# Optimization experiments

Hardware: AMD Instinct MI355X
Metric: run time of the kernel (lower is better)

The kernel has to match this reference:

```python
import jax, jax.numpy as jnp
import numpy as np

D = 256      # wsi_projection_dim / SNN hidden
E = 1024     # wsi_embedding_dim
N = 60000    # num WSI patches
H = 8        # n_heads
DH = D // H  # head dim
K = 3        # int(6 * topk_ratio)
SIZES = (100, 200, 300, 400, 500, 600)
NC = 4       # num_classes
EPS = 1e-5


def _ln(x, g, b):
    m = x.mean(-1, keepdims=True)
    v = ((x - m) ** 2).mean(-1, keepdims=True)
    return (x - m) / jnp.sqrt(v + EPS) * g + b


def setup_inputs() -> dict:
    key = jax.random.key(0)
    ks = iter(jax.random.split(key, 64))
    sc = 0.02
    inp = {}
    inp["x_path"] = jax.random.normal(next(ks), (1, N, E), dtype=jnp.float32)
    for i, s in enumerate(SIZES):
        inp[f"x_omic{i+1}"] = jax.random.normal(next(ks), (s,), dtype=jnp.float32)
    # per-pathway SNN blocks: Linear(size,256)+ELU, Linear(256,256)+ELU
    for i, s in enumerate(SIZES):
        inp[f"sw1_{i}"] = sc * jax.random.normal(next(ks), (s, D), dtype=jnp.float32)
    inp["sb1"] = jnp.zeros((len(SIZES), D), jnp.float32)
    inp["sw2"] = sc * jax.random.normal(next(ks), (len(SIZES), D, D), dtype=jnp.float32)
    inp["sb2"] = jnp.zeros((len(SIZES), D), jnp.float32)
    # wsi projection
    inp["wp"] = sc * jax.random.normal(next(ks), (E, D), dtype=jnp.float32)
    inp["bp"] = jnp.zeros((D,), jnp.float32)
    # gene attention MLP 256->64->1
    inp["wa1"] = sc * jax.random.normal(next(ks), (D, 64), dtype=jnp.float32)
    inp["ba1"] = jnp.zeros((64,), jnp.float32)
    inp["wa2"] = sc * jax.random.normal(next(ks), (64, 1), dtype=jnp.float32)
    inp["ba2"] = jnp.zeros((1,), jnp.float32)
    # MultiheadAttention projections
    for nm in ("wq", "wk", "wv", "wo"):
        inp[nm] = sc * jax.random.normal(next(ks), (D, D), dtype=jnp.float32)
    for nm in ("bq", "bk", "bv", "bo"):
        inp[nm] = jnp.zeros((D,), jnp.float32)
    inp["ln1_g"] = jnp.ones((D,), jnp.float32)
    inp["ln1_b"] = jnp.zeros((D,), jnp.float32)
    # bilinear fusion 512->256->256
    inp["wf1"] = sc * jax.random.normal(next(ks), (2 * D, D), dtype=jnp.float32)
    inp["bf1"] = jnp.zeros((D,), jnp.float32)
    inp["wf2"] = sc * jax.random.normal(next(ks), (D, D), dtype=jnp.float32)
    inp["bf2"] = jnp.zeros((D,), jnp.float32)
    inp["ln2_g"] = jnp.ones((D,), jnp.float32)
    inp["ln2_b"] = jnp.zeros((D,), jnp.float32)
    inp["wc"] = sc * jax.random.normal(next(ks), (D, NC), dtype=jnp.float32)
    inp["bc"] = jnp.zeros((NC,), jnp.float32)
    return inp


def _forward(x_path, x_omics, sw1s, sb1, sw2, sb2, wp, bp, wa1, ba1, wa2, ba2,
             wq, bq, wk, bk, wv, bv, wo, bo, ln1_g, ln1_b,
             wf1, bf1, wf2, bf2, ln2_g, ln2_b, wc, bc):
    # per-pathway SNN (eval: AlphaDropout = identity)
    h = [jax.nn.elu(jax.nn.elu(x @ w1 + sb1[i]) @ sw2[i] + sb2[i])
         for i, (x, w1) in enumerate(zip(x_omics, sw1s))]
    bag = jnp.stack(h)[None]                      # [1, G, D]
    # gene selection: softmax -> topk -> gather (mask*gather == gather)
    scores = (jax.nn.relu(bag @ wa1 + ba1) @ wa2 + ba2)[..., 0]   # [1, G]
    attw = jax.nn.softmax(scores, axis=1)
    _, idx = jax.lax.top_k(attw, K)               # [1, K]
    selected = jnp.take_along_axis(bag, idx[..., None], axis=1)  # [1, K, D]
    # wsi projection (eval: Dropout = identity)
    wsi = jax.nn.relu(x_path @ wp + bp)           # [1, N, D]
    # cross-attention: queries = selected genes, keys/values = wsi patches
    q = (selected @ wq + bq).reshape(1, K, H, DH).transpose(0, 2, 1, 3)
    k_ = (wsi @ wk + bk).reshape(1, N, H, DH).transpose(0, 2, 1, 3)
    v_ = (wsi @ wv + bv).reshape(1, N, H, DH).transpose(0, 2, 1, 3)
    att = jax.nn.softmax(jnp.einsum('bhqd,bhkd->bhqk', q, k_) / np.float32(np.sqrt(DH)), axis=-1)
    attn_out = jnp.einsum('bhqk,bhkd->bhqd', att, v_).transpose(0, 2, 1, 3).reshape(1, K, D)
    attn_out = attn_out @ wo + bo                 # [1, K, D]
    # adaptive_avg_pool2d over N -> K bins (N divisible by K -> equal bins)
    pooled = wsi.reshape(1, K, N // K, D).mean(axis=2)  # [1, K, D]
    attended = _ln(attn_out + pooled, ln1_g, ln1_b)
    attended_mean = attended.mean(axis=1)         # [1, D]
    gene_features = selected.mean(axis=1)         # [1, D]
    comb = jnp.concatenate([attended_mean, gene_features], axis=1)  # [1, 2D]
    f = jax.nn.relu(comb @ wf1 + bf1)
    f = jax.nn.relu(f @ wf2 + bf2)
    fused = _ln(f + attended_mean, ln2_g, ln2_b)
    return fused @ wc + bc                        # [1, num_classes]


def reference(x_path, x_omic1, x_omic2, x_omic3, x_omic4, x_omic5, x_omic6,
              sw1_0, sw1_1, sw1_2, sw1_3, sw1_4, sw1_5, sb1, sw2, sb2,
              wp, bp, wa1, ba1, wa2, ba2,
              wq, bq, wk, bk, wv, bv, wo, bo, ln1_g, ln1_b,
              wf1, bf1, wf2, bf2, ln2_g, ln2_b, wc, bc):
    x_omics = (x_omic1, x_omic2, x_omic3, x_omic4, x_omic5, x_omic6)
    sw1s = (sw1_0, sw1_1, sw1_2, sw1_3, sw1_4, sw1_5)
    return _forward(x_path, x_omics, sw1s, sb1, sw2, sb2, wp, bp, wa1, ba1, wa2, ba2,
                    wq, bq, wk, bk, wv, bv, wo, bo, ln1_g, ln1_b,
                    wf1, bf1, wf2, bf2, ln2_g, ln2_b, wc, bc)
```

## Files before the change

### kernel.cpp

```cpp
#include <hip/hip_runtime.h>
#include <hip/hip_bf16.h>
#include <math.h>

typedef unsigned short ushort_t;
typedef __attribute__((ext_vector_type(8))) short bf16x8;
typedef __attribute__((ext_vector_type(4))) float f32x4;

#define NB 512
#define NBLK 469
#define TP 128
#define NHQ 24
#define LN_EPS 1e-5f

#define WS_BAG 0
#define WS_SEL 1536
#define WS_GENE 2304
#define WS_PM 3584
#define WS_PL (WS_PM + NB*NHQ)
#define WS_PACC (WS_PL + NB*NHQ)
#define WS_PPOOL (WS_PACC + NB*768)
#define WS_ATTN (WS_PPOOL + NB*768)
#define WS_POOLED (WS_ATTN + 768)
#define WS_BF16 (WS_POOLED + 768)
#define U_WPT 0
#define U_WKT 262144
#define U_WVT 327680
#define U_QB  393216

__device__ __forceinline__ ushort_t f2bf(float f) {
    __hip_bfloat16 h = __float2bfloat16(f);
    return *reinterpret_cast<ushort_t*>(&h);
}
__device__ __forceinline__ float bf2f(unsigned int u) {
    union { unsigned int i; float f; } c; c.i = u << 16; return c.f;
}
__device__ __forceinline__ unsigned int pk2(float a, float b) {
    return (unsigned int)f2bf(a) | ((unsigned int)f2bf(b) << 16);
}

__global__ void prep_kernel(const float* __restrict__ wp, const float* __restrict__ wk,
                            const float* __restrict__ wv, ushort_t* __restrict__ ub) {
    const int b = blockIdx.x, t = threadIdx.x;
    if (b < 16) {
        const int D16 = b;
        for (int i = 0; i < 64; ++i) {
            int f = t + i * 256;
            int K32 = f >> 9, r = f & 511;
            int lg = r >> 7, lm2 = (r >> 3) & 15, e = r & 7;
            int k = K32 * 32 + lg * 8 + e, d = D16 * 16 + lm2;
            ub[U_WPT + D16 * 16384 + f] = f2bf(wp[(size_t)k * 256 + d]);
        }
    } else if (b < 32) {
        const int D16 = b - 16;
        for (int i = 0; i < 16; ++i) {
            int f = t + i * 256;
            int K32 = f >> 9, r = f & 511;
            int lg = r >> 7, lm2 = (r >> 3) & 15, e = r & 7;
            int k = K32 * 32 + lg * 8 + e, d = D16 * 16 + lm2;
            ub[U_WKT + D16 * 4096 + f] = f2bf(wk[(size_t)k * 256 + d]);
        }
    } else {
        const int D16 = b - 32;
        for (int i = 0; i < 16; ++i) {
            int f = t + i * 256;
            int K32 = f >> 9, r = f & 511;
            int lg = r >> 7, lm2 = (r >> 3) & 15, e = r & 7;
            int k = K32 * 32 + lg * 8 + e, d = D16 * 16 + lm2;
            ub[U_WVT + D16 * 4096 + f] = f2bf(wv[(size_t)k * 256 + d]);
        }
    }
}

struct PrepArgs {
    const float* xo[6];
    const float* w1[6];
    int sz[6];
};

__global__ void snn_kernel(PrepArgs pa, const float* __restrict__ sb1,
                           const float* __restrict__ sw2, const float* __restrict__ sb2,
                           float* __restrict__ bag) {
    __shared__ float xsh[600];
    __shared__ float t1sh[256];
    const int i = blockIdx.x;
    const int t = threadIdx.x;
    const int s = pa.sz[i];
    const float* xo = pa.xo[i];
    const float* w1 = pa.w1[i];
    for (int j = t; j < s; j += 256) xsh[j] = xo[j];
    __syncthreads();
    float acc = sb1[i * 256 + t];
    for (int j = 0; j < s; ++j) acc += xsh[j] * w1[j * 256 + t];
    t1sh[t] = acc > 0.f ? acc : expm1f(acc);
    __syncthreads();
    float acc2 = sb2[i * 256 + t];
    const float* w2 = sw2 + (size_t)i * 256 * 256;
    for (int j = 0; j < 256; ++j) acc2 += t1sh[j] * w2[j * 256 + t];
    bag[i * 256 + t] = acc2 > 0.f ? acc2 : expm1f(acc2);
}

__global__ void select_kernel(const float* __restrict__ wa1, const float* __restrict__ ba1,
                              const float* __restrict__ wa2, const float* __restrict__ ba2,
                              const float* __restrict__ wq, const float* __restrict__ bq,
                              float* __restrict__ wsf, ushort_t* __restrict__ ub) {
    __shared__ float bsh[6][256];
    __shared__ float ysh[64];
    __shared__ float ssh[8];
    __shared__ int isel[3];
    const int t = threadIdx.x;
    for (int j = t; j < 1536; j += 256) ((float*)bsh)[j] = wsf[WS_BAG + j];
    __syncthreads();
    for (int i = 0; i < 6; ++i) {
        if (t < 64) {
            float acc = ba1[t];
            for (int j = 0; j < 256; ++j) acc += bsh[i][j] * wa1[j * 64 + t];
            ysh[t] = fmaxf(acc, 0.f) * wa2[t];
        }
        __syncthreads();
        if (t == 0) {
            float sc = ba2[0];
            for (int j = 0; j < 64; ++j) sc += ysh[j];
            ssh[i] = sc;
        }
        __syncthreads();
    }
    if (t == 0) {
        float sc[6];
        for (int i = 0; i < 6; ++i) sc[i] = ssh[i];
        for (int k = 0; k < 3; ++k) {
            int best = 0; float bv = sc[0];
            for (int i = 1; i < 6; ++i) if (sc[i] > bv) { bv = sc[i]; best = i; }
            isel[k] = best;
            sc[best] = -INFINITY;
        }
    }
    __syncthreads();
    float g = 0.f;
    for (int k = 0; k < 3; ++k) {
        float v = bsh[isel[k]][t];
        wsf[WS_SEL + k * 256 + t] = v;
        g += v;
    }
    wsf[WS_GENE + t] = g * (1.f / 3.f);
    for (int kq = 0; kq < 3; ++kq) {
        float acc = bq[t];
        const float* srow = bsh[isel[kq]];
        for (int j = 0; j < 256; ++j) acc += srow[j] * wq[j * 256 + t];
        float v = acc * 0.17677669529663687f;
        int hq = (t >> 5) * 3 + kq, dd = t & 31;
        ub[U_QB + hq * 32 + dd] = f2bf(v);
    }
}

#define LOAD_X(xr, c) { \
    _Pragma("unroll") for (int i_ = 0; i_ < 4; ++i_) { \
        int f_ = tid + i_ * 512; int p_ = f_ >> 4, c4_ = f_ & 15; \
        if (n0 + p_ < 60000) \
            xr[i_] = *(const float4*)(xp + (size_t)(n0 + p_) * 1024 + (c) * 64 + c4_ * 4); \
        else { xr[i_].x = 0.f; xr[i_].y = 0.f; xr[i_].z = 0.f; xr[i_].w = 0.f; } } }

#define STORE_X(xr) { \
    _Pragma("unroll") for (int i_ = 0; i_ < 4; ++i_) { \
        int f_ = tid + i_ * 512; int p_ = f_ >> 4, c4_ = f_ & 15; \
        int byte_ = (p_ * 128 + c4_ * 8) ^ ((p_ & 7) << 4); \
        uint2 u_; u_.x = pk2(xr[i_].x, xr[i_].y); u_.y = pk2(xr[i_].z, xr[i_].w); \
        *(uint2*)((char*)x_s + byte_) = u_; } }

#define LOAD_W1(dst, c) { \
    _Pragma("unroll") for (int ks_ = 0; ks_ < 2; ++ks_) \
    _Pragma("unroll") for (int dt_ = 0; dt_ < 4; ++dt_) \
        dst[ks_ * 4 + dt_] = *(const bf16x8*)(wpP + ((size_t)(((w & 3) * 4 + dt_) * 32 + (c) * 2 + ks_)) * 512 + lane * 8); }

#define MFMA_CHUNK(wf) { \
    _Pragma("unroll") for (int ks_ = 0; ks_ < 2; ++ks_) { \
        bf16x8 bfr_[4]; \
        _Pragma("unroll") for (int pt_ = 0; pt_ < 4; ++pt_) { \
            int p_ = wp0 + pt_ * 16 + lm; \
            int byte_ = (p_ * 128 + ks_ * 64 + lg * 16) ^ ((p_ & 7) << 4); \
            bfr_[pt_] = *(const bf16x8*)((const char*)x_s + byte_); } \
        _Pragma("unroll") for (int dt_ = 0; dt_ < 4; ++dt_) \
        _Pragma("unroll") for (int pt_ = 0; pt_ < 4; ++pt_) \
            acc[dt_ * 4 + pt_] = __builtin_amdgcn_mfma_f32_16x16x32_bf16(wf[ks_ * 4 + dt_], bfr_[pt_], acc[dt_ * 4 + pt_], 0, 0, 0); } }

__global__ __launch_bounds__(512, 2) void main_kernel(
    const float* __restrict__ xp, const float* __restrict__ bp,
    const float* __restrict__ bk, const float* __restrict__ bv,
    const ushort_t* __restrict__ ub, float* __restrict__ wsf)
{
    __shared__ __align__(16) ushort_t wsi_s[128 * 256];
    __shared__ __align__(16) ushort_t kv_s[128 * 256];
    __shared__ __align__(16) ushort_t x_s[128 * 64];
    __shared__ __align__(16) ushort_t p_s[NHQ * 128];
    __shared__ float mlc_s[72];

    const int tid = threadIdx.x;
    const int b = blockIdx.x;
    const int lane = tid & 63;
    const int w = tid >> 6;
    const int lm = lane & 15;
    const int lg = lane >> 4;
    const int lmc = (lm < 3) ? lm : 2;
    const int wd0 = (w & 3) * 64;
    const int wp0 = (w >> 2) * 64;

    const ushort_t* wpP = ub + U_WPT;
    const ushort_t* wkP = ub + U_WKT;
    const ushort_t* wvP = ub + U_WVT;

    bf16x8 qfrag;
    if (lm < 3) qfrag = *(const bf16x8*)(ub + U_QB + (w * 3 + lm) * 32 + lg * 8);
    else { bf16x8 z = {0,0,0,0,0,0,0,0}; qfrag = z; }

    if (tid < 24) { mlc_s[tid] = -INFINITY; mlc_s[24 + tid] = 0.f; mlc_s[48 + tid] = 0.f; }

    f32x4 pv[2] = {{0.f,0.f,0.f,0.f},{0.f,0.f,0.f,0.f}};
    float pl0 = 0.f, pl1 = 0.f, pl2 = 0.f;
    __syncthreads();

    const int n0 = b * TP;
    {
        f32x4 acc[16];
#pragma unroll
        for (int i = 0; i < 16; ++i) acc[i] = (f32x4){0.f,0.f,0.f,0.f};

        float4 xr[4];
        bf16x8 wA[8], wB[8];
        LOAD_X(xr, 0); LOAD_W1(wA, 0);
        for (int c = 0; c < 16; c += 2) {
            __syncthreads();
            STORE_X(xr);
            __syncthreads();
            LOAD_X(xr, c + 1); LOAD_W1(wB, c + 1);
            MFMA_CHUNK(wA);
            __syncthreads();
            STORE_X(xr);
            __syncthreads();
            if (c + 2 < 16) { LOAD_X(xr, c + 2); LOAD_W1(wA, c + 2); }
            MFMA_CHUNK(wB);
        }
#pragma unroll
        for (int dt = 0; dt < 4; ++dt) {
            int d0 = wd0 + dt * 16 + lg * 4;
            float4 bb = *(const float4*)(bp + d0);
#pragma unroll
            for (int pt = 0; pt < 4; ++pt) {
                int p = wp0 + pt * 16 + lm;
                f32x4 v = acc[dt * 4 + pt];
                uint2 u;
                u.x = pk2(fmaxf(v[0] + bb.x, 0.f), fmaxf(v[1] + bb.y, 0.f));
                u.y = pk2(fmaxf(v[2] + bb.z, 0.f), fmaxf(v[3] + bb.w, 0.f));
                int byte = (p * 512 + d0 * 2) ^ ((p & 7) << 4);
                *(uint2*)((char*)wsi_s + byte) = u;
            }
        }
    }
    __syncthreads();

    {
        int d = tid & 255, half = tid >> 8;
#pragma unroll 16
        for (int pp = 0; pp < 64; ++pp) {
            int p = half * 64 + pp;
            int gp = n0 + p;
            int byte = (p * 512 + d * 2) ^ ((p & 7) << 4);
            float v = bf2f((unsigned int)*(const ushort_t*)((const char*)wsi_s + byte));
            pl0 += (gp < 20000) ? v : 0.f;
            pl1 += (gp >= 20000 && gp < 40000) ? v : 0.f;
            pl2 += (gp >= 40000 && gp < 60000) ? v : 0.f;
        }
    }

    {
        f32x4 acc2[16];
#pragma unroll
        for (int i = 0; i < 16; ++i) acc2[i] = (f32x4){0.f,0.f,0.f,0.f};
#pragma unroll
        for (int ks = 0; ks < 8; ++ks) {
            bf16x8 wf[4];
#pragma unroll
            for (int dt = 0; dt < 4; ++dt)
                wf[dt] = *(const bf16x8*)(wkP + ((size_t)(((w & 3) * 4 + dt) * 8 + ks)) * 512 + lane * 8);
            bf16x8 bfr[4];
#pragma unroll
            for (int pt = 0; pt < 4; ++pt) {
                int p = wp0 + pt * 16 + lm;
                int byte = (p * 512 + (ks * 32 + lg * 8) * 2) ^ ((p & 7) << 4);
                bfr[pt] = *(const bf16x8*)((const char*)wsi_s + byte);
            }
#pragma unroll
            for (int dt = 0; dt < 4; ++dt)
#pragma unroll
                for (int pt = 0; pt < 4; ++pt)
                    acc2[dt * 4 + pt] = __builtin_amdgcn_mfma_f32_16x16x32_bf16(wf[dt], bfr[pt], acc2[dt * 4 + pt], 0, 0, 0);
        }
#pragma unroll
        for (int dt = 0; dt < 4; ++dt) {
            int d0 = wd0 + dt * 16 + lg * 4;
            float4 bb = *(const float4*)(bk + d0);
#pragma unroll
            for (int pt = 0; pt < 4; ++pt) {
                int p = wp0 + pt * 16 + lm;
                f32x4 v = acc2[dt * 4 + pt];
                uint2 u;
                u.x = pk2(v[0] + bb.x, v[1] + bb.y);
                u.y = pk2(v[2] + bb.z, v[3] + bb.w);
                int byte = (p * 512 + d0 * 2) ^ ((p & 7) << 4);
                *(uint2*)((char*)kv_s + byte) = u;
            }
        }
    }
    __syncthreads();

    {
        f32x4 sc[8];
#pragma unroll
        for (int blk = 0; blk < 8; ++blk) {
            sc[blk] = (f32x4){0.f,0.f,0.f,0.f};
            int p = blk * 16 + lm;
            int byte = (p * 512 + (w * 32 + lg * 8) * 2) ^ ((p & 7) << 4);
            bf16x8 kf = *(const bf16x8*)((const char*)kv_s + byte);
            sc[blk] = __builtin_amdgcn_mfma_f32_16x16x32_bf16(kf, qfrag, sc[blk], 0, 0, 0);
        }
        float m_old = mlc_s[w * 3 + lmc];
        float tmax = -INFINITY;
#pragma unroll
        for (int blk = 0; blk < 8; ++blk)
#pragma unroll
            for (int j = 0; j < 4; ++j) {
                int p = blk * 16 + lg * 4 + j;
                if (n0 + p >= 60000) sc[blk][j] = -INFINITY;
                tmax = fmaxf(tmax, sc[blk][j]);
            }
        tmax = fmaxf(tmax, __shfl_xor(tmax, 16));
        tmax = fmaxf(tmax, __shfl_xor(tmax, 32));
        float mnew = fmaxf(m_old, tmax);
        float lsum = 0.f;
#pragma unroll
        for (int blk = 0; blk < 8; ++blk)
#pragma unroll
            for (int j = 0; j < 4; ++j) {
                float e = __expf(sc[blk][j] - mnew);
                sc[blk][j] = e;
                lsum += e;
            }
        lsum += __shfl_xor(lsum, 16);
        lsum += __shfl_xor(lsum, 32);
        float corr = __expf(m_old - mnew);
        if (lane < 3) {
            mlc_s[w * 3 + lane] = mnew;
            mlc_s[24 + w * 3 + lane] = mlc_s[24 + w * 3 + lane] * corr + lsum;
            mlc_s[48 + w * 3 + lane] = corr;
        }
        if (lm < 3) {
#pragma unroll
            for (int blk = 0; blk < 8; ++blk) {
                int p0 = blk * 16 + lg * 4;
                *(unsigned int*)(p_s + (w * 3 + lm) * 128 + p0) = pk2(sc[blk][0], sc[blk][1]);
                *(unsigned int*)(p_s + (w * 3 + lm) * 128 + p0 + 2) = pk2(sc[blk][2], sc[blk][3]);
            }
        }
    }
    __syncthreads();

    {
        f32x4 acc2[16];
#pragma unroll
        for (int i = 0; i < 16; ++i) acc2[i] = (f32x4){0.f,0.f,0.f,0.f};
#pragma unroll
        for (int ks = 0; ks < 8; ++ks) {
            bf16x8 wf[4];
#pragma unroll
            for (int dt = 0; dt < 4; ++dt)
                wf[dt] = *(const bf16x8*)(wvP + ((size_t)(((w & 3) * 4 + dt) * 8 + ks)) * 512 + lane * 8);
            bf16x8 bfr[4];
#pragma unroll
            for (int pt = 0; pt < 4; ++pt) {
                int p = wp0 + pt * 16 + lm;
                int byte = (p * 512 + (ks * 32 + lg * 8) * 2) ^ ((p & 7) << 4);
                bfr[pt] = *(const bf16x8*)((const char*)wsi_s + byte);
            }
#pragma unroll
            for (int dt = 0; dt < 4; ++dt)
#pragma unroll
                for (int pt = 0; pt < 4; ++pt)
                    acc2[dt * 4 + pt] = __builtin_amdgcn_mfma_f32_16x16x32_bf16(wf[dt], bfr[pt], acc2[dt * 4 + pt], 0, 0, 0);
        }
#pragma unroll
        for (int dt = 0; dt < 4; ++dt) {
            int d0 = wd0 + dt * 16 + lg * 4;
            float4 bb = *(const float4*)(bv + d0);
#pragma unroll
            for (int pt = 0; pt < 4; ++pt) {
                int p = wp0 + pt * 16 + lm;
                f32x4 v = acc2[dt * 4 + pt];
                float r[4] = {v[0] + bb.x, v[1] + bb.y, v[2] + bb.z, v[3] + bb.w};
#pragma unroll
                for (int j = 0; j < 4; ++j) {
                    int dd = d0 + j;
                    int byte = (dd * 256 + p * 2) ^ ((dd & 7) << 4);
                    *(ushort_t*)((char*)kv_s + byte) = f2bf(r[j]);
                }
            }
        }
    }
    __syncthreads();

    {
        float cj[4];
#pragma unroll
        for (int j = 0; j < 4; ++j) {
            int q = lg * 4 + j;
            cj[j] = mlc_s[48 + w * 3 + (q < 3 ? q : 2)];
        }
#pragma unroll
        for (int nb = 0; nb < 2; ++nb)
#pragma unroll
            for (int j = 0; j < 4; ++j) pv[nb][j] *= cj[j];
#pragma unroll
        for (int ks = 0; ks < 4; ++ks) {
            bf16x8 pa = *(const bf16x8*)(p_s + (w * 3 + lmc) * 128 + ks * 32 + lg * 8);
#pragma unroll
            for (int nb = 0; nb < 2; ++nb) {
                int row = w * 32 + nb * 16 + lm;
                int byte = (row * 256 + (ks * 32 + lg * 8) * 2) ^ ((row & 7) << 4);
                bf16x8 vb = *(const bf16x8*)((const char*)kv_s + byte);
                pv[nb] = __builtin_amdgcn_mfma_f32_16x16x32_bf16(pa, vb, pv[nb], 0, 0, 0);
            }
        }
    }

    __syncthreads();
    {
        float* scr = (float*)x_s;
        int d = tid & 255, half = tid >> 8;
        scr[half * 768 + 0 * 256 + d] = pl0;
        scr[half * 768 + 1 * 256 + d] = pl1;
        scr[half * 768 + 2 * 256 + d] = pl2;
    }
    __syncthreads();
    if (tid < 256) {
        float* scr = (float*)x_s;
#pragma unroll
        for (int bin = 0; bin < 3; ++bin)
            wsf[WS_PPOOL + b * 768 + bin * 256 + tid] = scr[bin * 256 + tid] + scr[768 + bin * 256 + tid];
    }
    if (tid < 24) {
        wsf[WS_PM + b * 24 + tid] = mlc_s[tid];
        wsf[WS_PL + b * 24 + tid] = mlc_s[24 + tid];
    }
    if (lg == 0) {
#pragma unroll
        for (int nb = 0; nb < 2; ++nb)
#pragma unroll
            for (int j = 0; j < 3; ++j) {
                int hq = w * 3 + j, dd = nb * 16 + lm;
                wsf[WS_PACC + b * 768 + hq * 32 + dd] = pv[nb][j];
            }
    }
}

__global__ void combine_kernel(float* __restrict__ wsf) {
    const int bidx = blockIdx.x;
    const int t = threadIdx.x;
    if (bidx < NHQ) {
        const int hq = bidx;
        float lmx = -INFINITY;
        for (int b = t; b < NBLK; b += 64) lmx = fmaxf(lmx, wsf[WS_PM + b * 24 + hq]);
#pragma unroll
        for (int o = 32; o > 0; o >>= 1) lmx = fmaxf(lmx, __shfl_xor(lmx, o));
        const float M = lmx;
        float L = 0.f;
        for (int b = t; b < NBLK; b += 64)
            L += wsf[WS_PL + b * 24 + hq] * __expf(wsf[WS_PM + b * 24 + hq] - M);
#pragma unroll
        for (int o = 32; o > 0; o >>= 1) L += __shfl_xor(L, o);
        const int dd = t & 31, half = t >> 5;
        float O = 0.f;
        for (int b = half; b < NBLK; b += 2)
            O += wsf[WS_PACC + b * 768 + hq * 32 + dd] * __expf(wsf[WS_PM + b * 24 + hq] - M);
        O += __shfl_xor(O, 32);
        if (t < 32) {
            int h = hq / 3, kq = hq - h * 3;
            wsf[WS_ATTN + kq * 256 + h * 32 + dd] = O / L;
        }
    } else {
        const int bin = bidx - NHQ;
        for (int rep = 0; rep < 4; ++rep) {
            int d = rep * 64 + t;
            float s = 0.f;
            for (int b = 0; b < NBLK; ++b) s += wsf[WS_PPOOL + b * 768 + bin * 256 + d];
            wsf[WS_POOLED + bin * 256 + d] = s * (1.f / 20000.f);
        }
    }
}

__device__ __forceinline__ float block_sum256(float v, float* red, int t) {
#pragma unroll
    for (int o = 32; o > 0; o >>= 1) v += __shfl_xor(v, o);
    if ((t & 63) == 0) red[t >> 6] = v;
    __syncthreads();
    float r = red[0] + red[1] + red[2] + red[3];
    __syncthreads();
    return r;
}

__global__ void final_kernel(const float* __restrict__ wo, const float* __restrict__ bo,
                             const float* __restrict__ ln1g, const float* __restrict__ ln1b,
                             const float* __restrict__ wf1, const float* __restrict__ bf1,
                             const float* __restrict__ wf2, const float* __restrict__ bf2,
                             const float* __restrict__ ln2g, const float* __restrict__ ln2b,
                             const float* __restrict__ wc, const float* __restrict__ bc,
                             float* __restrict__ wsf, float* __restrict__ out) {
    __shared__ float attnC[3][256];
    __shared__ float att[3][256];
    __shared__ float amean[256];
    __shared__ float gf[256];
    __shared__ float f1[256];
    __shared__ float red[256];
    const int t = threadIdx.x;
    for (int j = t; j < 768; j += 256) ((float*)attnC)[j] = wsf[WS_ATTN + j];
    gf[t] = wsf[WS_GENE + t];
    __syncthreads();
    for (int kq = 0; kq < 3; ++kq) {
        float acc = bo[t];
        for (int j = 0; j < 256; ++j) acc += attnC[kq][j] * wo[j * 256 + t];
        float x = acc + wsf[WS_POOLED + kq * 256 + t];
        float m = block_sum256(x, red, t) * (1.f / 256.f);
        float dv = x - m;
        float var = block_sum256(dv * dv, red, t) * (1.f / 256.f);
        att[kq][t] = dv * rsqrtf(var + LN_EPS) * ln1g[t] + ln1b[t];
    }
    __syncthreads();
    amean[t] = (att[0][t] + att[1][t] + att[2][t]) * (1.f / 3.f);
    __syncthreads();
    {
        float acc = bf1[t];
        for (int j = 0; j < 256; ++j) acc += amean[j] * wf1[j * 256 + t];
        for (int j = 0; j < 256; ++j) acc += gf[j] * wf1[(256 + j) * 256 + t];
        f1[t] = fmaxf(acc, 0.f);
    }
    __syncthreads();
    float acc2 = bf2[t];
    for (int j = 0; j < 256; ++j) acc2 += f1[j] * wf2[j * 256 + t];
    float y = fmaxf(acc2, 0.f) + amean[t];
    float m2 = block_sum256(y, red, t) * (1.f / 256.f);
    float dv2 = y - m2;
    float v2 = block_sum256(dv2 * dv2, red, t) * (1.f / 256.f);
    float fused = dv2 * rsqrtf(v2 + LN_EPS) * ln2g[t] + ln2b[t];
    red[t] = fused;
    __syncthreads();
    if (t < 4) {
        float o = bc[t];
        for (int j = 0; j < 256; ++j) o += red[j] * wc[j * 4 + t];
        out[t] = o;
    }
}

extern "C" void kernel_launch(void* const* d_in, const int* in_sizes, int n_in,
                              void* d_out, int out_size, void* d_ws, size_t ws_size,
                              hipStream_t stream) {
    const float* xp = (const float*)d_in[0];
    PrepArgs pa;
    for (int i = 0; i < 6; ++i) {
        pa.xo[i] = (const float*)d_in[1 + i];
        pa.w1[i] = (const float*)d_in[7 + i];
        pa.sz[i] = in_sizes[1 + i];
    }
    const float* sb1 = (const float*)d_in[13];
    const float* sw2 = (const float*)d_in[14];
    const float* sb2 = (const float*)d_in[15];
    const float* wp  = (const float*)d_in[16];
    const float* bp  = (const float*)d_in[17];
    const float* wa1 = (const float*)d_in[18];
    const float* ba1 = (const float*)d_in[19];
    const float* wa2 = (const float*)d_in[20];
    const float* ba2 = (const float*)d_in[21];
    const float* wq  = (const float*)d_in[22];
    const float* wk  = (const float*)d_in[23];
    const float* wv  = (const float*)d_in[24];
    const float* wo  = (const float*)d_in[25];
    const float* bq  = (const float*)d_in[26];
    const float* bk  = (const float*)d_in[27];
    const float* bv  = (const float*)d_in[28];
    const float* bo  = (const float*)d_in[29];
    const float* ln1g = (const float*)d_in[30];
    const float* ln1b = (const float*)d_in[31];
    const float* wf1 = (const float*)d_in[32];
    const float* bf1 = (const float*)d_in[33];
    const float* wf2 = (const float*)d_in[34];
    const float* bf2 = (const float*)d_in[35];
    const float* ln2g = (const float*)d_in[36];
    const float* ln2b = (const float*)d_in[37];
    const float* wc  = (const float*)d_in[38];
    const float* bc  = (const float*)d_in[39];

    float* wsf = (float*)d_ws;
    float* out = (float*)d_out;
    ushort_t* ub = (ushort_t*)(wsf + WS_BF16);

    prep_kernel<<<dim3(48), dim3(256), 0, stream>>>(wp, wk, wv, ub);
    snn_kernel<<<dim3(6), dim3(256), 0, stream>>>(pa, sb1, sw2, sb2, wsf + WS_BAG);
    select_kernel<<<dim3(1), dim3(256), 0, stream>>>(wa1, ba1, wa2, ba2, wq, bq, wsf, ub);
    main_kernel<<<dim3(NBLK), dim3(512), 0, stream>>>(xp, bp, bk, bv, ub, wsf);
    combine_kernel<<<dim3(27), dim3(64), 0, stream>>>(wsf);
    final_kernel<<<dim3(1), dim3(256), 0, stream>>>(wo, bo, ln1g, ln1b, wf1, bf1, wf2, bf2,
                                                    ln2g, ln2b, wc, bc, wsf, out);
}
```

Measured before the change: 740.6 us.

## Split fused projection/attention kernel into proj, attn and pool kernels

Replaces the single fused main kernel with three kernels: a projection GEMM that writes the ReLU'd bf16 WSI projection to workspace in an MFMA-friendly layout, an attention kernel over 64-patch tiles that computes K/V and partial softmax, and a separate pooling reduction. This aims to raise occupancy and parallelism, since the fused kernel had heavy register and LDS use and only 469 blocks. In exchange it adds a round trip of roughly 30 MB through global memory and more launches, and it runs only when the workspace is large enough. The LDS swizzle in the fallback path is also changed.

```diff
diff --git a/kernel.cpp b/kernel.cpp
--- a/kernel.cpp
+++ b/kernel.cpp
@@ -6,26 +6,28 @@
 typedef __attribute__((ext_vector_type(8))) short bf16x8;
 typedef __attribute__((ext_vector_type(4))) float f32x4;
 
-#define NB 512
-#define NBLK 469
-#define TP 128
 #define NHQ 24
 #define LN_EPS 1e-5f
+#define NBLK_F 469
+#define NBLK_A 938
+#define NPOOL 256
 
 #define WS_BAG 0
 #define WS_SEL 1536
 #define WS_GENE 2304
 #define WS_PM 3584
-#define WS_PL (WS_PM + NB*NHQ)
-#define WS_PACC (WS_PL + NB*NHQ)
-#define WS_PPOOL (WS_PACC + NB*768)
-#define WS_ATTN (WS_PPOOL + NB*768)
-#define WS_POOLED (WS_ATTN + 768)
-#define WS_BF16 (WS_POOLED + 768)
+#define WS_PL 28160
+#define WS_PACC 52736
+#define WS_PPOOL 839168
+#define WS_ATTN 1232384
+#define WS_POOLED 1233152
+#define WS_BF16 1233920
 #define U_WPT 0
 #define U_WKT 262144
 #define U_WVT 327680
 #define U_QB  393216
+#define U_WSIP 401408
+#define WS_SPLIT_BYTES 36474880ULL
 
 __device__ __forceinline__ ushort_t f2bf(float f) {
     __hip_bfloat16 h = __float2bfloat16(f);
@@ -152,6 +154,324 @@
     }
 }
 
+
+#define PLOAD_X(xr, c) { \
+    _Pragma("unroll") for (int i_ = 0; i_ < 4; ++i_) { \
+        int f_ = tid + i_ * 512; int p_ = f_ >> 4, c4_ = f_ & 15; \
+        if (n0 + p_ < 60000) \
+            xr[i_] = *(const float4*)(xp + (size_t)(n0 + p_) * 1024 + (c) * 64 + c4_ * 4); \
+        else { xr[i_].x = 0.f; xr[i_].y = 0.f; xr[i_].z = 0.f; xr[i_].w = 0.f; } } }
+
+#define PSTORE_X(xr, buf) { \
+    _Pragma("unroll") for (int i_ = 0; i_ < 4; ++i_) { \
+        int f_ = tid + i_ * 512; int p_ = f_ >> 4, c4_ = f_ & 15; \
+        int byte_ = (p_ * 128 + c4_ * 8) ^ ((p_ & 7) << 4); \
+        uint2 u_; u_.x = pk2(xr[i_].x, xr[i_].y); u_.y = pk2(xr[i_].z, xr[i_].w); \
+        *(uint2*)((buf) + byte_) = u_; } }
+
+__global__ __launch_bounds__(512, 4) void proj_kernel(
+    const float* __restrict__ xp, const float* __restrict__ bp,
+    const ushort_t* __restrict__ ub, ushort_t* __restrict__ wsiP)
+{
+    __shared__ __align__(16) char xbuf[2][16384];
+    const int tid = threadIdx.x;
+    const int b = blockIdx.x;
+    const int lane = tid & 63;
+    const int w = tid >> 6;
+    const int lm = lane & 15;
+    const int lg = lane >> 4;
+    const int wd0 = (w & 3) * 64;
+    const int n0 = b * 128;
+    const ushort_t* wpP = ub + U_WPT;
+
+    f32x4 acc[16];
+#pragma unroll
+    for (int i = 0; i < 16; ++i) acc[i] = (f32x4){0.f, 0.f, 0.f, 0.f};
+
+    float4 xr[4];
+    PLOAD_X(xr, 0);
+    PSTORE_X(xr, xbuf[0]);
+    PLOAD_X(xr, 1);
+    __syncthreads();
+#pragma unroll 1
+    for (int c = 0; c < 16; ++c) {
+        const char* cur = xbuf[c & 1];
+        if (c < 15) PSTORE_X(xr, xbuf[(c + 1) & 1]);
+        if (c < 14) PLOAD_X(xr, c + 2);
+#pragma unroll
+        for (int ks = 0; ks < 2; ++ks) {
+            bf16x8 wf[4];
+#pragma unroll
+            for (int dt = 0; dt < 4; ++dt)
+                wf[dt] = *(const bf16x8*)(wpP + ((size_t)(((w & 3) * 4 + dt) * 32 + c * 2 + ks)) * 512 + lane * 8);
+            bf16x8 bfr[4];
+#pragma unroll
+            for (int pt = 0; pt < 4; ++pt) {
+                int p = (w >> 2) * 64 + pt * 16 + lm;
+                int byte = (p * 128 + ks * 64 + lg * 16) ^ ((p & 7) << 4);
+                bfr[pt] = *(const bf16x8*)(cur + byte);
+            }
+#pragma unroll
+            for (int dt = 0; dt < 4; ++dt)
+#pragma unroll
+                for (int pt = 0; pt < 4; ++pt)
+                    acc[dt * 4 + pt] = __builtin_amdgcn_mfma_f32_16x16x32_bf16(wf[dt], bfr[pt], acc[dt * 4 + pt], 0, 0, 0);
+        }
+        __syncthreads();
+    }
+#pragma unroll
+    for (int dt = 0; dt < 4; ++dt) {
+        int d0 = wd0 + dt * 16 + lg * 4;
+        float4 bb = *(const float4*)(bp + d0);
+        int ks2 = d0 >> 5, lg2 = (d0 >> 3) & 3, e0 = d0 & 7;
+#pragma unroll
+        for (int pt = 0; pt < 4; ++pt) {
+            int p16 = b * 8 + (w >> 2) * 4 + pt;
+            f32x4 v = acc[dt * 4 + pt];
+            uint2 u;
+            u.x = pk2(fmaxf(v[0] + bb.x, 0.f), fmaxf(v[1] + bb.y, 0.f));
+            u.y = pk2(fmaxf(v[2] + bb.z, 0.f), fmaxf(v[3] + bb.w, 0.f));
+            *(uint2*)(wsiP + (size_t)((p16 * 8 + ks2) * 4 + lg2) * 128 + lm * 8 + e0) = u;
+        }
+    }
+}
+
+__global__ __launch_bounds__(256, 4) void attn_kernel(
+    const float* __restrict__ bk, const float* __restrict__ bv,
+    const ushort_t* __restrict__ ub, const ushort_t* __restrict__ wsiP,
+    float* __restrict__ wsf)
+{
+    __shared__ __align__(16) ushort_t kv_s[64 * 256];
+    __shared__ __align__(16) ushort_t p_s[24 * 64];
+    const int tid = threadIdx.x;
+    const int b = blockIdx.x;
+    const int lane = tid & 63, w = tid >> 6;
+    const int lm = lane & 15, lg = lane >> 4;
+    const int lmc = lm < 3 ? lm : 2;
+    const int n0 = b * 64;
+    const int wd0 = w * 64;
+    const ushort_t* wkP = ub + U_WKT;
+    const ushort_t* wvP = ub + U_WVT;
+
+    {
+        f32x4 acc[16];
+#pragma unroll
+        for (int i = 0; i < 16; ++i) acc[i] = (f32x4){0.f, 0.f, 0.f, 0.f};
+#pragma unroll
+        for (int ks = 0; ks < 8; ++ks) {
+            bf16x8 wf[4], bfr[4];
+#pragma unroll
+            for (int dt = 0; dt < 4; ++dt)
+                wf[dt] = *(const bf16x8*)(wkP + ((size_t)((w * 4 + dt) * 8 + ks)) * 512 + lane * 8);
+#pragma unroll
+            for (int pt = 0; pt < 4; ++pt)
+                bfr[pt] = *(const bf16x8*)(wsiP + (size_t)(((b * 4 + pt) * 8 + ks) * 4 + lg) * 128 + lm * 8);
+#pragma unroll
+            for (int dt = 0; dt < 4; ++dt)
+#pragma unroll
+                for (int pt = 0; pt < 4; ++pt)
+                    acc[dt * 4 + pt] = __builtin_amdgcn_mfma_f32_16x16x32_bf16(wf[dt], bfr[pt], acc[dt * 4 + pt], 0, 0, 0);
+        }
+#pragma unroll
+        for (int dt = 0; dt < 4; ++dt) {
+            int d0 = wd0 + dt * 16 + lg * 4;
+            float4 bb = *(const float4*)(bk + d0);
+#pragma unroll
+            for (int pt = 0; pt < 4; ++pt) {
+                int p = pt * 16 + lm;
+                f32x4 v = acc[dt * 4 + pt];
+                uint2 u;
+                u.x = pk2(v[0] + bb.x, v[1] + bb.y);
+                u.y = pk2(v[2] + bb.z, v[3] + bb.w);
+                int byte = (p * 512 + d0 * 2) ^ ((p & 7) << 4);
+                *(uint2*)((char*)kv_s + byte) = u;
+            }
+        }
+    }
+    __syncthreads();
+
+    float m_reg[2], l_reg[2];
+#pragma unroll
+    for (int hh = 0; hh < 2; ++hh) {
+        int h = w * 2 + hh;
+        bf16x8 qf;
+        if (lm < 3) qf = *(const bf16x8*)(ub + U_QB + (h * 3 + lm) * 32 + lg * 8);
+        else { bf16x8 z = {0,0,0,0,0,0,0,0}; qf = z; }
+        f32x4 sc[4];
+#pragma unroll
+        for (int blk = 0; blk < 4; ++blk) {
+            sc[blk] = (f32x4){0.f, 0.f, 0.f, 0.f};
+            int p = blk * 16 + lm;
+            int byte = (p * 512 + (h * 32 + lg * 8) * 2) ^ ((p & 7) << 4);
+            bf16x8 kf = *(const bf16x8*)((const char*)kv_s + byte);
+            sc[blk] = __builtin_amdgcn_mfma_f32_16x16x32_bf16(kf, qf, sc[blk], 0, 0, 0);
+        }
+        float tmax = -INFINITY;
+#pragma unroll
+        for (int blk = 0; blk < 4; ++blk)
+#pragma unroll
+            for (int j = 0; j < 4; ++j) {
+                int p = blk * 16 + lg * 4 + j;
+                if (n0 + p >= 60000) sc[blk][j] = -INFINITY;
+                tmax = fmaxf(tmax, sc[blk][j]);
+            }
+        tmax = fmaxf(tmax, __shfl_xor(tmax, 16));
+        tmax = fmaxf(tmax, __shfl_xor(tmax, 32));
+        float lsum = 0.f;
+#pragma unroll
+        for (int blk = 0; blk < 4; ++blk)
+#pragma unroll
+            for (int j = 0; j < 4; ++j) {
+                float e = __expf(sc[blk][j] - tmax);
+                sc[blk][j] = e;
+                lsum += e;
+            }
+        lsum += __shfl_xor(lsum, 16);
+        lsum += __shfl_xor(lsum, 32);
+        m_reg[hh] = tmax;
+        l_reg[hh] = lsum;
+        if (lm < 3) {
+#pragma unroll
+            for (int blk = 0; blk < 4; ++blk) {
+                int p0 = blk * 16 + lg * 4;
+                *(unsigned int*)(p_s + (h * 3 + lm) * 64 + p0) = pk2(sc[blk][0], sc[blk][1]);
+                *(unsigned int*)(p_s + (h * 3 + lm) * 64 + p0 + 2) = pk2(sc[blk][2], sc[blk][3]);
+            }
+        }
+    }
+    __syncthreads();
+
+    {
+        f32x4 acc[16];
+#pragma unroll
+        for (int i = 0; i < 16; ++i) acc[i] = (f32x4){0.f, 0.f, 0.f, 0.f};
+#pragma unroll
+        for (int ks = 0; ks < 8; ++ks) {
+            bf16x8 wf[4], bfr[4];
+#pragma unroll
+            for (int dt = 0; dt < 4; ++dt)
+                wf[dt] = *(const bf16x8*)(wvP + ((size_t)((w * 4 + dt) * 8 + ks)) * 512 + lane * 8);
+#pragma unroll
+            for (int pt = 0; pt < 4; ++pt)
+                bfr[pt] = *(const bf16x8*)(wsiP + (size_t)(((b * 4 + pt) * 8 + ks) * 4 + lg) * 128 + lm * 8);
+#pragma unroll
+            for (int dt = 0; dt < 4; ++dt)
+#pragma unroll
+                for (int pt = 0; pt < 4; ++pt)
+                    acc[dt * 4 + pt] = __builtin_amdgcn_mfma_f32_16x16x32_bf16(wf[dt], bfr[pt], acc[dt * 4 + pt], 0, 0, 0);
+        }
+        __syncthreads();
+#pragma unroll
+        for (int dt = 0; dt < 4; ++dt) {
+            int d0 = wd0 + dt * 16 + lg * 4;
+            float4 bb = *(const float4*)(bv + d0);
+#pragma unroll
+            for (int pt = 0; pt < 4; ++pt) {
+                int p = pt * 16 + lm;
+                f32x4 v = acc[dt * 4 + pt];
+                float r[4] = {v[0] + bb.x, v[1] + bb.y, v[2] + bb.z, v[3] + bb.w};
+#pragma unroll
+                for (int j = 0; j < 4; ++j) {
+                    int dd = d0 + j;
+                    int byte = (dd * 128 + p * 2) ^ ((dd & 7) << 4);
+                    *(ushort_t*)((char*)kv_s + byte) = f2bf(r[j]);
+                }
+            }
+        }
+    }
+    __syncthreads();
+
+    f32x4 pv[2][2];
+#pragma unroll
+    for (int hh = 0; hh < 2; ++hh)
+#pragma unroll
+        for (int nb = 0; nb < 2; ++nb) pv[hh][nb] = (f32x4){0.f, 0.f, 0.f, 0.f};
+#pragma unroll
+    for (int hh = 0; hh < 2; ++hh) {
+        int h = w * 2 + hh;
+#pragma unroll
+        for (int ks = 0; ks < 2; ++ks) {
+            bf16x8 pa = *(const bf16x8*)(p_s + (h * 3 + lmc) * 64 + ks * 32 + lg * 8);
+#pragma unroll
+            for (int nb = 0; nb < 2; ++nb) {
+                int row = h * 32 + nb * 16 + lm;
+                int byte = (row * 128 + (ks * 32 + lg * 8) * 2) ^ ((row & 7) << 4);
+                bf16x8 vb = *(const bf16x8*)((const char*)kv_s + byte);
+                pv[hh][nb] = __builtin_amdgcn_mfma_f32_16x16x32_bf16(pa, vb, pv[hh][nb], 0, 0, 0);
+            }
+        }
+    }
+
+    if (lg == 0) {
+#pragma unroll
+        for (int hh = 0; hh < 2; ++hh)
+#pragma unroll
+            for (int nb = 0; nb < 2; ++nb)
+#pragma unroll
+                for (int j = 0; j < 3; ++j) {
+                    int hq = (w * 2 + hh) * 3 + j;
+                    wsf[WS_PACC + b * 768 + hq * 32 + nb * 16 + lm] = pv[hh][nb][j];
+                }
+    }
+    if (lm < 3 && lg == 0) {
+#pragma unroll
+        for (int hh = 0; hh < 2; ++hh) {
+            int hq = (w * 2 + hh) * 3 + lm;
+            wsf[WS_PM + b * 24 + hq] = m_reg[hh];
+            wsf[WS_PL + b * 24 + hq] = l_reg[hh];
+        }
+    }
+}
+
+__global__ __launch_bounds__(256, 8) void pool_kernel(const ushort_t* __restrict__ wsiP,
+                                                      float* __restrict__ wsf) {
+    const int tid = threadIdx.x, b = blockIdx.x;
+    const int lane = tid & 63;
+    const int lm = lane & 15, lg = (lane >> 4) & 3;
+    const int ks = ((b * 4) + (tid >> 6)) & 7;
+    f32x4 s[3][2];
+#pragma unroll
+    for (int i = 0; i < 3; ++i) { s[i][0] = (f32x4){0,0,0,0}; s[i][1] = (f32x4){0,0,0,0}; }
+    for (int sl = b * 256 + tid; sl < 1921024; sl += 65536) {
+        int p16 = sl >> 9;
+        if (p16 >= 3750) continue;
+        uint4 u = *(const uint4*)(wsiP + (size_t)sl * 8);
+        int bin = (p16 >= 2500) ? 2 : (p16 >= 1250 ? 1 : 0);
+        f32x4 a, c;
+        a[0] = bf2f(u.x & 0xffffu); a[1] = bf2f(u.x >> 16);
+        a[2] = bf2f(u.y & 0xffffu); a[3] = bf2f(u.y >> 16);
+        c[0] = bf2f(u.z & 0xffffu); c[1] = bf2f(u.z >> 16);
+        c[2] = bf2f(u.w & 0xffffu); c[3] = bf2f(u.w >> 16);
+        s[bin][0] += a; s[bin][1] += c;
+    }
+#pragma unroll
+    for (int o = 1; o < 16; o <<= 1)
+#pragma unroll
+        for (int bin = 0; bin < 3; ++bin)
+#pragma unroll
+            for (int hv = 0; hv < 2; ++hv)
+#pragma unroll
+                for (int e = 0; e < 4; ++e)
+                    s[bin][hv][e] += __shfl_xor(s[bin][hv][e], o);
+    if (lm == 0) {
+        int dbase = ks * 32 + lg * 8;
+#pragma unroll
+        for (int bin = 0; bin < 3; ++bin)
+#pragma unroll
+            for (int hv = 0; hv < 2; ++hv)
+#pragma unroll
+                for (int e = 0; e < 4; ++e)
+                    wsf[WS_PPOOL + b * 768 + bin * 256 + dbase + hv * 4 + e] = s[bin][hv][e];
+    } else if (lm == 1) {
+        int dbase = (ks ^ 4) * 32 + lg * 8;
+#pragma unroll
+        for (int bin = 0; bin < 3; ++bin)
+#pragma unroll
+            for (int e = 0; e < 8; ++e)
+                wsf[WS_PPOOL + b * 768 + bin * 256 + dbase + e] = 0.f;
+    }
+}
+
 #define LOAD_X(xr, c) { \
     _Pragma("unroll") for (int i_ = 0; i_ < 4; ++i_) { \
         int f_ = tid + i_ * 512; int p_ = f_ >> 4, c4_ = f_ & 15; \
@@ -217,12 +537,11 @@
     float pl0 = 0.f, pl1 = 0.f, pl2 = 0.f;
     __syncthreads();
 
-    const int n0 = b * TP;
+    const int n0 = b * 128;
     {
         f32x4 acc[16];
 #pragma unroll
         for (int i = 0; i < 16; ++i) acc[i] = (f32x4){0.f,0.f,0.f,0.f};
-
         float4 xr[4];
         bf16x8 wA[8], wB[8];
         LOAD_X(xr, 0); LOAD_W1(wA, 0);
@@ -397,7 +716,7 @@
 #pragma unroll
                 for (int j = 0; j < 4; ++j) {
                     int dd = d0 + j;
-                    int byte = (dd * 256 + p * 2) ^ ((dd & 7) << 4);
+                    int byte = (dd * 256 + p * 2) ^ ((dd & 14) << 2);
                     *(ushort_t*)((char*)kv_s + byte) = f2bf(r[j]);
                 }
             }
@@ -422,7 +741,7 @@
 #pragma unroll
             for (int nb = 0; nb < 2; ++nb) {
                 int row = w * 32 + nb * 16 + lm;
-                int byte = (row * 256 + (ks * 32 + lg * 8) * 2) ^ ((row & 7) << 4);
+                int byte = (row * 256 + (ks * 32 + lg * 8) * 2) ^ ((row & 14) << 2);
                 bf16x8 vb = *(const bf16x8*)((const char*)kv_s + byte);
                 pv[nb] = __builtin_amdgcn_mfma_f32_16x16x32_bf16(pa, vb, pv[nb], 0, 0, 0);
             }
@@ -459,24 +778,24 @@
     }
 }
 
-__global__ void combine_kernel(float* __restrict__ wsf) {
+__global__ void combine_kernel(float* __restrict__ wsf, int nblk, int npool) {
     const int bidx = blockIdx.x;
     const int t = threadIdx.x;
     if (bidx < NHQ) {
         const int hq = bidx;
         float lmx = -INFINITY;
-        for (int b = t; b < NBLK; b += 64) lmx = fmaxf(lmx, wsf[WS_PM + b * 24 + hq]);
+        for (int b = t; b < nblk; b += 64) lmx = fmaxf(lmx, wsf[WS_PM + b * 24 + hq]);
 #pragma unroll
         for (int o = 32; o > 0; o >>= 1) lmx = fmaxf(lmx, __shfl_xor(lmx, o));
         const float M = lmx;
         float L = 0.f;
-        for (int b = t; b < NBLK; b += 64)
+        for (int b = t; b < nblk; b += 64)
             L += wsf[WS_PL + b * 24 + hq] * __expf(wsf[WS_PM + b * 24 + hq] - M);
 #pragma unroll
         for (int o = 32; o > 0; o >>= 1) L += __shfl_xor(L, o);
         const int dd = t & 31, half = t >> 5;
         float O = 0.f;
-        for (int b = half; b < NBLK; b += 2)
+        for (int b = half; b < nblk; b += 2)
             O += wsf[WS_PACC + b * 768 + hq * 32 + dd] * __expf(wsf[WS_PM + b * 24 + hq] - M);
         O += __shfl_xor(O, 32);
         if (t < 32) {
@@ -488,7 +807,7 @@
         for (int rep = 0; rep < 4; ++rep) {
             int d = rep * 64 + t;
             float s = 0.f;
-            for (int b = 0; b < NBLK; ++b) s += wsf[WS_PPOOL + b * 768 + bin * 256 + d];
+            for (int b = 0; b < npool; ++b) s += wsf[WS_PPOOL + b * 768 + bin * 256 + d];
             wsf[WS_POOLED + bin * 256 + d] = s * (1.f / 20000.f);
         }
     }
@@ -601,8 +920,17 @@
     prep_kernel<<<dim3(48), dim3(256), 0, stream>>>(wp, wk, wv, ub);
     snn_kernel<<<dim3(6), dim3(256), 0, stream>>>(pa, sb1, sw2, sb2, wsf + WS_BAG);
     select_kernel<<<dim3(1), dim3(256), 0, stream>>>(wa1, ba1, wa2, ba2, wq, bq, wsf, ub);
-    main_kernel<<<dim3(NBLK), dim3(512), 0, stream>>>(xp, bp, bk, bv, ub, wsf);
-    combine_kernel<<<dim3(27), dim3(64), 0, stream>>>(wsf);
+
+    if (ws_size >= WS_SPLIT_BYTES) {
+        ushort_t* wsiP = ub + U_WSIP;
+        proj_kernel<<<dim3(NBLK_F), dim3(512), 0, stream>>>(xp, bp, ub, wsiP);
+        attn_kernel<<<dim3(NBLK_A), dim3(256), 0, stream>>>(bk, bv, ub, wsiP, wsf);
+        pool_kernel<<<dim3(NPOOL), dim3(256), 0, stream>>>(wsiP, wsf);
+        combine_kernel<<<dim3(27), dim3(64), 0, stream>>>(wsf, NBLK_A, NPOOL);
+    } else {
+        main_kernel<<<dim3(NBLK_F), dim3(512), 0, stream>>>(xp, bp, bk, bv, ub, wsf);
+        combine_kernel<<<dim3(27), dim3(64), 0, stream>>>(wsf, NBLK_F, NBLK_F);
+    }
     final_kernel<<<dim3(1), dim3(256), 0, stream>>>(wo, bo, ln1g, ln1b, wf1, bf1, wf2, bf2,
                                                     ln2g, ln2b, wc, bc, wsf, out);
 }
```

New measurement: 963.3 us. 30.1% more time.
